# Performance work log

Measured on AMD Instinct MI355X. Metric: run time of the kernel, lower is better.

## Reference

```python
import jax, jax.numpy as jnp
import numpy as np

NEG_SLOPE = 0.2  # PyG GATConv default LeakyReLU slope


def _gat_layer(x, src, dst, n_nodes, W, a_src, a_dst, b, heads, out_ch):
    # x: [N, F_in] -> h: [N, H, C]
    h = (x @ W).reshape(n_nodes, heads, out_ch)
    # per-node attention contributions [N, H]
    al_s = jnp.sum(h * a_src[None], axis=-1)
    al_d = jnp.sum(h * a_dst[None], axis=-1)
    # per-edge logits [E, H]
    e = jax.nn.leaky_relu(al_s[src] + al_d[dst], negative_slope=NEG_SLOPE)
    # segment softmax over incoming edges of each destination node
    m = jax.ops.segment_max(e, dst, num_segments=n_nodes)
    ex = jnp.exp(e - m[dst])
    denom = jax.ops.segment_sum(ex, dst, num_segments=n_nodes)
    alpha = ex / (denom[dst] + 1e-16)
    # weighted scatter-aggregate of source features
    out = jax.ops.segment_sum(h[src] * alpha[:, :, None], dst, num_segments=n_nodes)
    return out.reshape(n_nodes, heads * out_ch) + b


def setup_inputs() -> dict:
    key = jax.random.key(0)
    ks = jax.random.split(key, 16)
    N, E, F_in, hid, H, n_cls = 50000, 800000, 128, 64, 4, 10
    s = 0.1
    return {
        "x": jax.random.normal(ks[0], (N, F_in), jnp.float32),
        "edge_index": jax.random.randint(ks[1], (2, E), 0, N, jnp.int64),
        "W1": jax.random.normal(ks[2], (F_in, H * hid), jnp.float32) * s,
        "a_src1": jax.random.normal(ks[3], (H, hid), jnp.float32) * s,
        "a_dst1": jax.random.normal(ks[4], (H, hid), jnp.float32) * s,
        "b1": jax.random.normal(ks[5], (H * hid,), jnp.float32) * s,
        "W2": jax.random.normal(ks[6], (H * hid, H * hid), jnp.float32) * s,
        "a_src2": jax.random.normal(ks[7], (H, hid), jnp.float32) * s,
        "a_dst2": jax.random.normal(ks[8], (H, hid), jnp.float32) * s,
        "b2": jax.random.normal(ks[9], (H * hid,), jnp.float32) * s,
        "W3": jax.random.normal(ks[10], (H * hid, n_cls), jnp.float32) * s,
        "a_src3": jax.random.normal(ks[11], (1, n_cls), jnp.float32) * s,
        "a_dst3": jax.random.normal(ks[12], (1, n_cls), jnp.float32) * s,
        "b3": jax.random.normal(ks[13], (n_cls,), jnp.float32) * s,
    }


def reference(x, edge_index, W1, a_src1, a_dst1, b1, W2, a_src2, a_dst2, b2,
              W3, a_src3, a_dst3, b3):
    N = x.shape[0]
    loops = jnp.arange(N, dtype=edge_index.dtype)
    src = jnp.concatenate([edge_index[0], loops])  # add self loops (PyG default)
    dst = jnp.concatenate([edge_index[1], loops])
    # layer 1: heads=4, concat -> [N, 256], ELU (dropout is a no-op in eval)
    h = jax.nn.elu(_gat_layer(x, src, dst, N, W1, a_src1, a_dst1, b1, 4, 64))
    # layer 2
    h = jax.nn.elu(_gat_layer(h, src, dst, N, W2, a_src2, a_dst2, b2, 4, 64))
    # layer 3: heads=1 -> [N, num_classes]
    h = _gat_layer(h, src, dst, N, W3, a_src3, a_dst3, b3, 1, 10)
    pooled = jnp.mean(h, axis=0, keepdims=True)  # [1, num_classes]
    return jax.nn.log_softmax(pooled, axis=1)
```

## Files before the change

### kernel.cpp

```cpp
#include <hip/hip_runtime.h>
#include <math.h>

#define NEG_SLOPE 0.2f

typedef __attribute__((ext_vector_type(8))) short bf16x8;
typedef __attribute__((ext_vector_type(4))) float f32x4;
typedef __attribute__((ext_vector_type(2))) float f32x2;
typedef unsigned short u16;
typedef __attribute__((ext_vector_type(4))) unsigned short u16x4;

__device__ __forceinline__ float b2f(u16 u) {
    return __uint_as_float(((unsigned)u) << 16);
}
__device__ __forceinline__ u16 f2b(float f) {
    unsigned u = __float_as_uint(f);
    unsigned r = (u + 0x7fffu + ((u >> 16) & 1u)) >> 16;
    return (u16)r;
}

__global__ void prep(const float* __restrict__ x, u16* __restrict__ x_bf, int n4,
                     const float* __restrict__ W1, u16* __restrict__ w1t,
                     const float* __restrict__ W2, u16* __restrict__ w2t,
                     int* __restrict__ zero_base, int nzero,
                     int B0, int B1, int B2) {
    int blk = blockIdx.x;
    if (blk < B0) {
        int i = blk * 256 + threadIdx.x;
        if (i < n4) {
            float4 v = *reinterpret_cast<const float4*>(&x[i * 4]);
            u16x4 o;
            o[0] = f2b(v.x); o[1] = f2b(v.y); o[2] = f2b(v.z); o[3] = f2b(v.w);
            *reinterpret_cast<u16x4*>(&x_bf[i * 4]) = o;
        }
    } else if (blk < B1) {
        int i = (blk - B0) * 256 + threadIdx.x;
        if (i < 128 * 256) {
            int m = i >> 7, k = i & 127;
            w1t[i] = f2b(W1[(size_t)k * 256 + m]);
        }
    } else if (blk < B2) {
        int i = (blk - B1) * 256 + threadIdx.x;
        if (i < 256 * 256) {
            int m = i >> 8, k = i & 255;
            w2t[i] = f2b(W2[(size_t)k * 256 + m]);
        }
    } else {
        int i = (blk - B2) * 256 + threadIdx.x;
        if (i < nzero) zero_base[i] = 0;
    }
}

__global__ __launch_bounds__(256) void gemm_mfma(
        const u16* __restrict__ A, const u16* __restrict__ Bt,
        u16* __restrict__ C, int N, int K, int M) {
    __shared__ u16 As[128 * 64];
    __shared__ u16 Bs[128 * 64];
    const int tid = threadIdx.x;
    const int lane = tid & 63;
    const int wid = tid >> 6;
    const int wr = wid >> 1, wc = wid & 1;
    const int row0 = blockIdx.x * 128;
    const int col0 = blockIdx.y * 128;
    f32x4 acc[4][4] = {};
    for (int k0 = 0; k0 < K; k0 += 64) {
        if (k0) __syncthreads();
#pragma unroll
        for (int i = 0; i < 4; ++i) {
            int chunk = i * 256 + tid;
            int row = chunk >> 3;
            int slot = chunk & 7;
            int grow = row0 + row; if (grow >= N) grow = N - 1;
            bf16x8 v = *reinterpret_cast<const bf16x8*>(&A[(size_t)grow * K + k0 + slot * 8]);
            int swz = (chunk & ~7) | (slot ^ (row & 7));
            *reinterpret_cast<bf16x8*>(&As[swz * 8]) = v;
        }
#pragma unroll
        for (int i = 0; i < 4; ++i) {
            int chunk = i * 256 + tid;
            int row = chunk >> 3;
            int slot = chunk & 7;
            int gcol = col0 + row;
            bf16x8 v = *reinterpret_cast<const bf16x8*>(&Bt[(size_t)gcol * K + k0 + slot * 8]);
            int swz = (chunk & ~7) | (slot ^ (row & 7));
            *reinterpret_cast<bf16x8*>(&Bs[swz * 8]) = v;
        }
        __syncthreads();
#pragma unroll
        for (int kk = 0; kk < 2; ++kk) {
            bf16x8 ax[4], bx[4];
#pragma unroll
            for (int m = 0; m < 4; ++m) {
                int row = wr * 64 + m * 16 + (lane & 15);
                int slot = kk * 4 + (lane >> 4);
                ax[m] = *reinterpret_cast<const bf16x8*>(&As[(row * 8 + (slot ^ (row & 7))) * 8]);
            }
#pragma unroll
            for (int n = 0; n < 4; ++n) {
                int row = wc * 64 + n * 16 + (lane & 15);
                int slot = kk * 4 + (lane >> 4);
                bx[n] = *reinterpret_cast<const bf16x8*>(&Bs[(row * 8 + (slot ^ (row & 7))) * 8]);
            }
#pragma unroll
            for (int m = 0; m < 4; ++m)
#pragma unroll
                for (int n = 0; n < 4; ++n)
                    acc[m][n] = __builtin_amdgcn_mfma_f32_16x16x32_bf16(
                        ax[m], bx[n], acc[m][n], 0, 0, 0);
        }
    }
    const int crow = row0 + wr * 64;
    const int ccol = col0 + wc * 64;
#pragma unroll
    for (int m = 0; m < 4; ++m)
#pragma unroll
        for (int n = 0; n < 4; ++n)
#pragma unroll
            for (int r = 0; r < 4; ++r) {
                int rg = crow + m * 16 + (lane >> 4) * 4 + r;
                int cg = ccol + n * 16 + (lane & 15);
                if (rg < N) C[(size_t)rg * M + cg] = f2b(acc[m][n][r]);
            }
}

__global__ __launch_bounds__(256) void compute_al_cast(
        const u16* __restrict__ h, const float* __restrict__ a_s,
        const float* __restrict__ a_d, int N,
        float* __restrict__ pq, float* __restrict__ al_d,
        unsigned* __restrict__ h8) {
    const int lane = threadIdx.x & 63;
    const int half = lane >> 5;
    const int l32 = lane & 31;
    int w = (blockIdx.x * blockDim.x + threadIdx.x) >> 6;
    int n = w * 2 + half;
    if (n >= N) return;
    const int head = l32 >> 3;
    const int c0 = l32 * 8;
    bf16x8 v = *reinterpret_cast<const bf16x8*>(&h[(size_t)n * 256 + c0]);
    const float* asf = a_s + head * 64 + (l32 & 7) * 8;
    const float* adf = a_d + head * 64 + (l32 & 7) * 8;
    float ss = 0.f, sd = 0.f;
    float f[8];
#pragma unroll
    for (int j = 0; j < 8; ++j) {
        f[j] = b2f((u16)v[j]);
        ss = fmaf(f[j], asf[j], ss);
        sd = fmaf(f[j], adf[j], sd);
    }
    int w0 = 0, w1 = 0;
    w0 = __builtin_amdgcn_cvt_pk_fp8_f32(f[0], f[1], w0, false);
    w0 = __builtin_amdgcn_cvt_pk_fp8_f32(f[2], f[3], w0, true);
    w1 = __builtin_amdgcn_cvt_pk_fp8_f32(f[4], f[5], w1, false);
    w1 = __builtin_amdgcn_cvt_pk_fp8_f32(f[6], f[7], w1, true);
    uint2 hw; hw.x = (unsigned)w0; hw.y = (unsigned)w1;
    *reinterpret_cast<uint2*>(&h8[(size_t)n * 64 + 2 * l32]) = hw;
#pragma unroll
    for (int m = 1; m < 8; m <<= 1) {
        ss += __shfl_xor(ss, m, 64);
        sd += __shfl_xor(sd, m, 64);
    }
    if ((l32 & 7) == 0) {
        f32x2 pv; pv.x = __expf(ss); pv.y = __expf(NEG_SLOPE * ss);
        *reinterpret_cast<f32x2*>(&pq[(size_t)n * 8 + head * 2]) = pv;
        al_d[n * 4 + head] = sd;
    }
}

__global__ __launch_bounds__(256) void bucket_hist(
        const int* __restrict__ dstI, int E, int Etot,
        int* __restrict__ bcnt, int NB) {
    __shared__ int h[512];
    int t = threadIdx.x;
    for (int j = t; j < NB; j += 256) h[j] = 0;
    __syncthreads();
    int base = blockIdx.x * 2048;
#pragma unroll
    for (int j = 0; j < 8; ++j) {
        int e = base + j * 256 + t;
        if (e < Etot) {
            int d = (e < E) ? dstI[e] : (e - E);
            atomicAdd(&h[d >> 7], 1);
        }
    }
    __syncthreads();
    for (int j = t; j < NB; j += 256)
        if (h[j]) atomicAdd(&bcnt[j], h[j]);
}

__global__ __launch_bounds__(512) void bucket_scan(
        const int* __restrict__ bcnt, int NB, int Etot,
        int* __restrict__ bbase, int* __restrict__ bcursor,
        int* __restrict__ rp, int N) {
    __shared__ int a[512], b[512];
    int t = threadIdx.x;
    a[t] = (t < NB) ? bcnt[t] : 0;
    __syncthreads();
    int* s = a; int* d = b;
    for (int ofs = 1; ofs < 512; ofs <<= 1) {
        d[t] = (t >= ofs) ? s[t] + s[t - ofs] : s[t];
        __syncthreads();
        int* tmp = s; s = d; d = tmp;
    }
    int excl = (t == 0) ? 0 : s[t - 1];
    if (t < NB) { bbase[t] = excl; bcursor[t] = excl; }
    if (t == NB) bbase[NB] = Etot;
    if (t == 0) rp[N] = Etot;
}

#define EPB 16
__global__ __launch_bounds__(256) void bin_scatter(
        const int* __restrict__ srcI, const int* __restrict__ dstI,
        int E, int Etot, int* __restrict__ bcursor,
        unsigned* __restrict__ binned, int NB) {
    __shared__ int cnt[512];
    int t = threadIdx.x;
    for (int j = t; j < NB; j += 256) cnt[j] = 0;
    __syncthreads();
    int base_e = blockIdx.x * (256 * EPB) + t;
    unsigned rec[EPB];
    int bkt[EPB];
#pragma unroll
    for (int j = 0; j < EPB; ++j) {
        int e = base_e + j * 256;
        bkt[j] = -1;
        if (e < Etot) {
            int s = (e < E) ? srcI[e] : (e - E);
            int d = (e < E) ? dstI[e] : (e - E);
            bkt[j] = d >> 7;
            rec[j] = ((unsigned)(d & 127) << 16) | (unsigned)s;
            atomicAdd(&cnt[bkt[j]], 1);
        }
    }
    __syncthreads();
    for (int j = t; j < NB; j += 256) {
        int c = cnt[j];
        cnt[j] = c ? atomicAdd(&bcursor[j], c) : 0;
    }
    __syncthreads();
#pragma unroll
    for (int j = 0; j < EPB; ++j)
        if (bkt[j] >= 0) {
            int pos = atomicAdd(&cnt[bkt[j]], 1);
            binned[pos] = rec[j];
        }
}

__global__ __launch_bounds__(256) void bucket_csr(
        const unsigned* __restrict__ binned, const int* __restrict__ bbase,
        int N, int* __restrict__ rp, u16* __restrict__ srcp) {
    int b = blockIdx.x;
    int start = bbase[b];
    int cnt = bbase[b + 1] - start;
    __shared__ int dcnt[128];
    __shared__ int dofs[128];
    __shared__ int wtot;
    int t = threadIdx.x;
    if (t < 128) dcnt[t] = 0;
    __syncthreads();
    for (int i = t; i < cnt; i += 256)
        atomicAdd(&dcnt[binned[start + i] >> 16], 1);
    __syncthreads();
    int v = 0, x = 0;
    if (t < 128) {
        v = dcnt[t];
        x = v;
#pragma unroll
        for (int ofs = 1; ofs < 64; ofs <<= 1) {
            int u = __shfl_up(x, ofs, 64);
            if ((t & 63) >= ofs) x += u;
        }
    }
    if (t == 63) wtot = x;
    __syncthreads();
    if (t >= 64 && t < 128) x += wtot;
    if (t < 128) {
        int abs0 = start + (x - v);
        int d = b * 128 + t;
        if (d < N) rp[d] = abs0;
        dofs[t] = abs0;
    }
    __syncthreads();
    for (int i = t; i < cnt; i += 256) {
        unsigned rec = binned[start + i];
        int pos = atomicAdd(&dofs[rec >> 16], 1);
        srcp[pos] = (u16)(rec & 0xFFFFu);
    }
}

template<bool ELU>
__global__ __launch_bounds__(256) void gat_fused_h4(
        const unsigned* __restrict__ h8, const float* __restrict__ pq,
        const float* __restrict__ al_d, const float* __restrict__ b,
        const int* __restrict__ rp, const u16* __restrict__ srcp,
        int N, u16* __restrict__ out) {
    const int lane = threadIdx.x & 63;
    const int head = lane >> 4;
    int w = (blockIdx.x * blockDim.x + threadIdx.x) >> 6;
    int nw = (gridDim.x * blockDim.x) >> 6;
    for (int d = w; d < N; d += nw) {
        int i = rp[d], end = rp[d + 1];
        float ald = al_d[d * 4 + head];
        float pb = __expf(ald);
        float qb = __expf(NEG_SLOPE * ald);
        float acc0 = 0.f, acc1 = 0.f, acc2 = 0.f, acc3 = 0.f, L = 0.f;

#define EDGE1(S) {                                                             \
        unsigned hv_ = h8[(unsigned)(S) * 64u + (unsigned)lane];               \
        f32x2 pv_ = *reinterpret_cast<const f32x2*>(                           \
            &pq[(unsigned)(S) * 8u + (unsigned)head * 2u]);                    \
        float t_ = pv_.x * pb;                                                 \
        float e_ = (t_ > 1.f) ? t_ : pv_.y * qb;                               \
        L += e_;                                                               \
        f32x2 lo_ = __builtin_amdgcn_cvt_pk_f32_fp8((int)hv_, false);          \
        f32x2 hi_ = __builtin_amdgcn_cvt_pk_f32_fp8((int)hv_, true);           \
        acc0 = fmaf(e_, lo_.x, acc0); acc1 = fmaf(e_, lo_.y, acc1);            \
        acc2 = fmaf(e_, hi_.x, acc2); acc3 = fmaf(e_, hi_.y, acc3); }

        for (; i < end && (i & 3); ++i) EDGE1(srcp[i]);
        for (; i + 8 <= end; i += 8) {
            u16x4 sa = *reinterpret_cast<const u16x4*>(&srcp[i]);
            u16x4 sb = *reinterpret_cast<const u16x4*>(&srcp[i + 4]);
            unsigned ss[8] = {sa[0], sa[1], sa[2], sa[3], sb[0], sb[1], sb[2], sb[3]};
            unsigned hv[8];
            f32x2 pv[8];
#pragma unroll
            for (int j = 0; j < 8; ++j) {
                hv[j] = h8[ss[j] * 64u + (unsigned)lane];
                pv[j] = *reinterpret_cast<const f32x2*>(
                    &pq[ss[j] * 8u + (unsigned)head * 2u]);
            }
#pragma unroll
            for (int j = 0; j < 8; ++j) {
                float t = pv[j].x * pb;
                float e = (t > 1.f) ? t : pv[j].y * qb;
                L += e;
                f32x2 lo = __builtin_amdgcn_cvt_pk_f32_fp8((int)hv[j], false);
                f32x2 hi = __builtin_amdgcn_cvt_pk_f32_fp8((int)hv[j], true);
                acc0 = fmaf(e, lo.x, acc0); acc1 = fmaf(e, lo.y, acc1);
                acc2 = fmaf(e, hi.x, acc2); acc3 = fmaf(e, hi.y, acc3);
            }
        }
        if (i + 4 <= end) {
            u16x4 sa = *reinterpret_cast<const u16x4*>(&srcp[i]);
            unsigned ss[4] = {sa[0], sa[1], sa[2], sa[3]};
            unsigned hv[4];
            f32x2 pv[4];
#pragma unroll
            for (int j = 0; j < 4; ++j) {
                hv[j] = h8[ss[j] * 64u + (unsigned)lane];
                pv[j] = *reinterpret_cast<const f32x2*>(
                    &pq[ss[j] * 8u + (unsigned)head * 2u]);
            }
#pragma unroll
            for (int j = 0; j < 4; ++j) {
                float t = pv[j].x * pb;
                float e = (t > 1.f) ? t : pv[j].y * qb;
                L += e;
                f32x2 lo = __builtin_amdgcn_cvt_pk_f32_fp8((int)hv[j], false);
                f32x2 hi = __builtin_amdgcn_cvt_pk_f32_fp8((int)hv[j], true);
                acc0 = fmaf(e, lo.x, acc0); acc1 = fmaf(e, lo.y, acc1);
                acc2 = fmaf(e, hi.x, acc2); acc3 = fmaf(e, hi.y, acc3);
            }
            i += 4;
        }
        for (; i < end; ++i) EDGE1(srcp[i]);
#undef EDGE1

        float inv = 1.f / (L + 1e-16f);
        float4 bb = *reinterpret_cast<const float4*>(&b[lane * 4]);
        float o0 = fmaf(acc0, inv, bb.x);
        float o1 = fmaf(acc1, inv, bb.y);
        float o2 = fmaf(acc2, inv, bb.z);
        float o3 = fmaf(acc3, inv, bb.w);
        if (ELU) {
            o0 = (o0 > 0.f) ? o0 : expm1f(o0);
            o1 = (o1 > 0.f) ? o1 : expm1f(o1);
            o2 = (o2 > 0.f) ? o2 : expm1f(o2);
            o3 = (o3 > 0.f) ? o3 : expm1f(o3);
        }
        u16x4 ov;
        ov[0] = f2b(o0); ov[1] = f2b(o1); ov[2] = f2b(o2); ov[3] = f2b(o3);
        *reinterpret_cast<u16x4*>(&out[(size_t)d * 256 + lane * 4]) = ov;
    }
}

__global__ __launch_bounds__(256) void compute_al3(
        const u16* __restrict__ ob, const float* __restrict__ W3,
        const float* __restrict__ as3, const float* __restrict__ ad3, int N,
        float* __restrict__ pq3, float* __restrict__ al_d) {
    __shared__ float was[256], wad[256];
    {
        int t = threadIdx.x;
        float ss = 0.f, sd = 0.f;
#pragma unroll
        for (int c = 0; c < 10; ++c) {
            float w = W3[t * 10 + c];
            ss = fmaf(w, as3[c], ss);
            sd = fmaf(w, ad3[c], sd);
        }
        was[t] = ss; wad[t] = sd;
    }
    __syncthreads();
    const int lane = threadIdx.x & 63;
    int n = (blockIdx.x * blockDim.x + threadIdx.x) >> 6;
    if (n >= N) return;
    u16x4 hv = *reinterpret_cast<const u16x4*>(&ob[(size_t)n * 256 + lane * 4]);
    float4 ws = *reinterpret_cast<const float4*>(&was[lane * 4]);
    float4 wd = *reinterpret_cast<const float4*>(&wad[lane * 4]);
    float f0 = b2f((u16)hv[0]), f1 = b2f((u16)hv[1]);
    float f2 = b2f((u16)hv[2]), f3 = b2f((u16)hv[3]);
    float ss = f0 * ws.x + f1 * ws.y + f2 * ws.z + f3 * ws.w;
    float sd = f0 * wd.x + f1 * wd.y + f2 * wd.z + f3 * wd.w;
#pragma unroll
    for (int m = 1; m < 64; m <<= 1) {
        ss += __shfl_xor(ss, m, 64);
        sd += __shfl_xor(sd, m, 64);
    }
    if (lane == 0) {
        f32x2 pv; pv.x = __expf(ss); pv.y = __expf(NEG_SLOPE * ss);
        *reinterpret_cast<f32x2*>(&pq3[(size_t)n * 2]) = pv;
        al_d[n] = sd;
    }
}

__global__ __launch_bounds__(256) void l3_edge(
        const float* __restrict__ pq3, const float* __restrict__ al_d,
        const int* __restrict__ rp, const u16* __restrict__ srcp,
        int N, float* __restrict__ wq) {
    const int lane = threadIdx.x & 63;
    int w = (blockIdx.x * blockDim.x + threadIdx.x) >> 6;
    int nw = (gridDim.x * blockDim.x) >> 6;
    for (int d = w; d < N; d += nw) {
        int start = rp[d], end = rp[d + 1];
        float ald = al_d[d];
        float pb = __expf(ald);
        float qb = __expf(NEG_SLOPE * ald);
        float L = 0.f;
        for (int i = start + lane; i < end; i += 64) {
            f32x2 pqv = *reinterpret_cast<const f32x2*>(&pq3[(unsigned)srcp[i] * 2u]);
            float t = pqv.x * pb;
            L += (t > 1.f) ? t : pqv.y * qb;
        }
#pragma unroll
        for (int m = 1; m < 64; m <<= 1) L += __shfl_xor(L, m, 64);
        float inv = 1.f / (L + 1e-16f);
        for (int i = start + lane; i < end; i += 64) {
            unsigned s = srcp[i];
            f32x2 pqv = *reinterpret_cast<const f32x2*>(&pq3[s * 2u]);
            float t = pqv.x * pb;
            float e = (t > 1.f) ? t : pqv.y * qb;
            atomicAdd(&wq[s], e * inv);
        }
    }
}

__global__ __launch_bounds__(256) void wcolsum(const u16* __restrict__ ob,
                                               const float* __restrict__ w, int N,
                                               float* __restrict__ pp) {
    __shared__ float sh[4][256];
    const int lane = threadIdx.x & 63;
    const int wid = threadIdx.x >> 6;
    int wv = (blockIdx.x * blockDim.x + threadIdx.x) >> 6;
    int nw = (gridDim.x * blockDim.x) >> 6;
    float a0 = 0.f, a1 = 0.f, a2 = 0.f, a3 = 0.f;
    for (int n = wv; n < N; n += nw) {
        float wn = w[n];
        u16x4 hv = *reinterpret_cast<const u16x4*>(&ob[(size_t)n * 256 + lane * 4]);
        a0 = fmaf(wn, b2f((u16)hv[0]), a0);
        a1 = fmaf(wn, b2f((u16)hv[1]), a1);
        a2 = fmaf(wn, b2f((u16)hv[2]), a2);
        a3 = fmaf(wn, b2f((u16)hv[3]), a3);
    }
    sh[wid][lane * 4 + 0] = a0;
    sh[wid][lane * 4 + 1] = a1;
    sh[wid][lane * 4 + 2] = a2;
    sh[wid][lane * 4 + 3] = a3;
    __syncthreads();
    int t = threadIdx.x;
    float s = sh[0][t] + sh[1][t] + sh[2][t] + sh[3][t];
    atomicAdd(&pp[t], s);
}

__global__ void final_out(const float* __restrict__ pp, const float* __restrict__ W3,
                          const float* __restrict__ b3, int N, float* __restrict__ out) {
    __shared__ float acc[10];
    int t = threadIdx.x;
    if (t < 10) acc[t] = 0.f;
    __syncthreads();
    float pk = pp[t] / (float)N;
#pragma unroll
    for (int c = 0; c < 10; ++c) atomicAdd(&acc[c], pk * W3[t * 10 + c]);
    __syncthreads();
    if (t == 0) {
        float p[10];
        float mx = -INFINITY;
        for (int c = 0; c < 10; ++c) {
            p[c] = acc[c] + b3[c];
            mx = fmaxf(mx, p[c]);
        }
        float s = 0.f;
        for (int c = 0; c < 10; ++c) s += expf(p[c] - mx);
        float ls = logf(s);
        for (int c = 0; c < 10; ++c) out[c] = p[c] - mx - ls;
    }
}

extern "C" void kernel_launch(void* const* d_in, const int* in_sizes, int n_in,
                              void* d_out, int out_size, void* d_ws, size_t ws_size,
                              hipStream_t stream) {
    const float* x   = (const float*)d_in[0];
    const int*   ei  = (const int*)d_in[1];
    const float* W1  = (const float*)d_in[2];
    const float* as1 = (const float*)d_in[3];
    const float* ad1 = (const float*)d_in[4];
    const float* b1  = (const float*)d_in[5];
    const float* W2  = (const float*)d_in[6];
    const float* as2 = (const float*)d_in[7];
    const float* ad2 = (const float*)d_in[8];
    const float* b2  = (const float*)d_in[9];
    const float* W3  = (const float*)d_in[10];
    const float* as3 = (const float*)d_in[11];
    const float* ad3 = (const float*)d_in[12];
    const float* b3  = (const float*)d_in[13];
    float* out = (float*)d_out;

    const int N = in_sizes[0] / 128;
    const int E = in_sizes[1] / 2;
    const int Etot = E + N;
    const int NB = (N + 127) >> 7;
    const int* srcI = ei;
    const int* dstI = ei + E;

    char* base = (char*)d_ws;
    size_t off = 0;
    auto alloc = [&](size_t bytes) {
        void* p = base + off;
        off = (off + bytes + 255) & ~(size_t)255;
        return p;
    };
    u16* x_bf  = (u16*)alloc((size_t)N * 128 * 2);
    u16* h_bf  = (u16*)alloc((size_t)N * 256 * 2);
    unsigned* h8 = (unsigned*)alloc((size_t)N * 256);
    u16* oa_bf = (u16*)alloc((size_t)N * 256 * 2);
    u16* ob_bf = (u16*)alloc((size_t)N * 256 * 2);
    u16* w1t   = (u16*)alloc(256 * 128 * 2);
    u16* w2t   = (u16*)alloc(256 * 256 * 2);
    float* pq   = (float*)alloc((size_t)N * 8 * 4);
    float* al_d = (float*)alloc((size_t)N * 4 * 4);
    float* pq3  = (float*)alloc((size_t)N * 2 * 4);
    int* bcnt   = (int*)alloc(512 * 4);
    float* wq   = (float*)alloc((size_t)N * 4);
    float* pp   = (float*)alloc(256 * 4);
    int* rp     = (int*)alloc((size_t)(N + 1) * 4);
    int* bbase  = (int*)alloc(512 * 4);
    int* bcursor = (int*)alloc(512 * 4);
    unsigned* binned = (unsigned*)alloc((size_t)Etot * 4);
    u16* srcp   = (u16*)alloc((size_t)Etot * 2);

    const int n4 = N * 128 / 4;
    const int B0 = (n4 + 255) / 256;
    const int B1 = B0 + (128 * 256 + 255) / 256;
    const int B2 = B1 + (256 * 256 + 255) / 256;
    int span = (int)(((char*)(pp + 256) - (char*)bcnt) / 4);
    const int B3 = B2 + (span + 255) / 256;
    prep<<<B3, 256, 0, stream>>>(x, x_bf, n4, W1, w1t, W2, w2t,
                                 bcnt, span, B0, B1, B2);

    bucket_hist<<<(Etot + 2047) / 2048, 256, 0, stream>>>(dstI, E, Etot, bcnt, NB);
    bucket_scan<<<1, 512, 0, stream>>>(bcnt, NB, Etot, bbase, bcursor, rp, N);
    bin_scatter<<<(Etot + 256 * EPB - 1) / (256 * EPB), 256, 0, stream>>>(
        srcI, dstI, E, Etot, bcursor, binned, NB);
    bucket_csr<<<NB, 256, 0, stream>>>(binned, bbase, N, rp, srcp);

    const int FUSED_BLOCKS = (N + 3) / 4;
    const int ALC_BLOCKS = (N / 2 + 3) / 4;
    const int GX = (N + 127) / 128;

    {
        dim3 g(GX, 2);
        gemm_mfma<<<g, 256, 0, stream>>>(x_bf, w1t, h_bf, N, 128, 256);
        compute_al_cast<<<ALC_BLOCKS, 256, 0, stream>>>(h_bf, as1, ad1, N,
                                                        pq, al_d, h8);
        gat_fused_h4<true><<<FUSED_BLOCKS, 256, 0, stream>>>(
            h8, pq, al_d, b1, rp, srcp, N, oa_bf);
    }
    {
        dim3 g(GX, 2);
        gemm_mfma<<<g, 256, 0, stream>>>(oa_bf, w2t, h_bf, N, 256, 256);
        compute_al_cast<<<ALC_BLOCKS, 256, 0, stream>>>(h_bf, as2, ad2, N,
                                                        pq, al_d, h8);
        gat_fused_h4<true><<<FUSED_BLOCKS, 256, 0, stream>>>(
            h8, pq, al_d, b2, rp, srcp, N, ob_bf);
    }
    {
        compute_al3<<<(N + 3) / 4, 256, 0, stream>>>(ob_bf, W3, as3, ad3, N, pq3, al_d);
        l3_edge<<<(N + 3) / 4, 256, 0, stream>>>(pq3, al_d, rp, srcp, N, wq);
        wcolsum<<<1024, 256, 0, stream>>>(ob_bf, wq, N, pp);
        final_out<<<1, 256, 0, stream>>>(pp, W3, b3, N, out);
    }
}
```

Before: 331.6 us.

## Fuse attention-logit and fp8 cast epilogue into GEMM; split edges across half-waves

The GEMM epilogue now computes the per-head source and destination attention dot products with shuffle reductions and writes the fp8 features directly. This removes the bf16 h round trip and the separate compute_al_cast kernel. The aggregation kernel is reorganised so that each half-wave takes alternate groups of edges, with each lane handling 8 channels using 8-byte fp8 loads. The two halves are combined with a cross-half shuffle at the end. The cost is byte-granular, scattered fp8 stores in the GEMM epilogue and extra shuffle work.

```diff
diff --git a/kernel.cpp b/kernel.cpp
--- a/kernel.cpp
+++ b/kernel.cpp
@@ -8,6 +8,7 @@
 typedef __attribute__((ext_vector_type(2))) float f32x2;
 typedef unsigned short u16;
 typedef __attribute__((ext_vector_type(4))) unsigned short u16x4;
+typedef __attribute__((ext_vector_type(8))) unsigned short u16x8;
 
 __device__ __forceinline__ float b2f(u16 u) {
     return __uint_as_float(((unsigned)u) << 16);
@@ -50,9 +51,12 @@
     }
 }
 
-__global__ __launch_bounds__(256) void gemm_mfma(
+__global__ __launch_bounds__(256) void gemm_mfma_fused(
         const u16* __restrict__ A, const u16* __restrict__ Bt,
-        u16* __restrict__ C, int N, int K, int M) {
+        int N, int K,
+        const float* __restrict__ a_s, const float* __restrict__ a_d,
+        unsigned char* __restrict__ h8b, float* __restrict__ pq,
+        float* __restrict__ al_d) {
     __shared__ u16 As[128 * 64];
     __shared__ u16 Bs[128 * 64];
     const int tid = threadIdx.x;
@@ -108,60 +112,45 @@
                         ax[m], bx[n], acc[m][n], 0, 0, 0);
         }
     }
+    const int head = blockIdx.y * 2 + wc;
+    float asf[4], adf[4];
+#pragma unroll
+    for (int n = 0; n < 4; ++n) {
+        asf[n] = a_s[head * 64 + n * 16 + (lane & 15)];
+        adf[n] = a_d[head * 64 + n * 16 + (lane & 15)];
+    }
     const int crow = row0 + wr * 64;
-    const int ccol = col0 + wc * 64;
-#pragma unroll
-    for (int m = 0; m < 4; ++m)
-#pragma unroll
-        for (int n = 0; n < 4; ++n)
-#pragma unroll
-            for (int r = 0; r < 4; ++r) {
-                int rg = crow + m * 16 + (lane >> 4) * 4 + r;
-                int cg = ccol + n * 16 + (lane & 15);
-                if (rg < N) C[(size_t)rg * M + cg] = f2b(acc[m][n][r]);
-            }
-}
-
-__global__ __launch_bounds__(256) void compute_al_cast(
-        const u16* __restrict__ h, const float* __restrict__ a_s,
-        const float* __restrict__ a_d, int N,
-        float* __restrict__ pq, float* __restrict__ al_d,
-        unsigned* __restrict__ h8) {
-    const int lane = threadIdx.x & 63;
-    const int half = lane >> 5;
-    const int l32 = lane & 31;
-    int w = (blockIdx.x * blockDim.x + threadIdx.x) >> 6;
-    int n = w * 2 + half;
-    if (n >= N) return;
-    const int head = l32 >> 3;
-    const int c0 = l32 * 8;
-    bf16x8 v = *reinterpret_cast<const bf16x8*>(&h[(size_t)n * 256 + c0]);
-    const float* asf = a_s + head * 64 + (l32 & 7) * 8;
-    const float* adf = a_d + head * 64 + (l32 & 7) * 8;
-    float ss = 0.f, sd = 0.f;
-    float f[8];
-#pragma unroll
-    for (int j = 0; j < 8; ++j) {
-        f[j] = b2f((u16)v[j]);
-        ss = fmaf(f[j], asf[j], ss);
-        sd = fmaf(f[j], adf[j], sd);
-    }
-    int w0 = 0, w1 = 0;
-    w0 = __builtin_amdgcn_cvt_pk_fp8_f32(f[0], f[1], w0, false);
-    w0 = __builtin_amdgcn_cvt_pk_fp8_f32(f[2], f[3], w0, true);
-    w1 = __builtin_amdgcn_cvt_pk_fp8_f32(f[4], f[5], w1, false);
-    w1 = __builtin_amdgcn_cvt_pk_fp8_f32(f[6], f[7], w1, true);
-    uint2 hw; hw.x = (unsigned)w0; hw.y = (unsigned)w1;
-    *reinterpret_cast<uint2*>(&h8[(size_t)n * 64 + 2 * l32]) = hw;
-#pragma unroll
-    for (int m = 1; m < 8; m <<= 1) {
-        ss += __shfl_xor(ss, m, 64);
-        sd += __shfl_xor(sd, m, 64);
-    }
-    if ((l32 & 7) == 0) {
-        f32x2 pv; pv.x = __expf(ss); pv.y = __expf(NEG_SLOPE * ss);
-        *reinterpret_cast<f32x2*>(&pq[(size_t)n * 8 + head * 2]) = pv;
-        al_d[n * 4 + head] = sd;
+#pragma unroll
+    for (int m = 0; m < 4; ++m) {
+#pragma unroll
+        for (int r = 0; r < 4; ++r) {
+            float ss = 0.f, sd = 0.f;
+#pragma unroll
+            for (int n = 0; n < 4; ++n) {
+                float v = acc[m][n][r];
+                ss = fmaf(v, asf[n], ss);
+                sd = fmaf(v, adf[n], sd);
+            }
+#pragma unroll
+            for (int msk = 1; msk < 16; msk <<= 1) {
+                ss += __shfl_xor(ss, msk, 64);
+                sd += __shfl_xor(sd, msk, 64);
+            }
+            int rg = crow + m * 16 + (lane >> 4) * 4 + r;
+            if (rg < N) {
+                if ((lane & 15) == 0) {
+                    f32x2 pv; pv.x = __expf(ss); pv.y = __expf(NEG_SLOPE * ss);
+                    *reinterpret_cast<f32x2*>(&pq[(size_t)rg * 8 + head * 2]) = pv;
+                    al_d[rg * 4 + head] = sd;
+                }
+#pragma unroll
+                for (int n = 0; n < 4; ++n) {
+                    int w8 = __builtin_amdgcn_cvt_pk_fp8_f32(acc[m][n][r], acc[m][n][r], 0, false);
+                    h8b[(size_t)rg * 256 + head * 64 + n * 16 + (lane & 15)] =
+                        (unsigned char)(w8 & 0xFF);
+                }
+            }
+        }
     }
 }
 
@@ -293,93 +282,96 @@
         const int* __restrict__ rp, const u16* __restrict__ srcp,
         int N, u16* __restrict__ out) {
     const int lane = threadIdx.x & 63;
-    const int head = lane >> 4;
+    const int hlf = lane >> 5;
+    const int l = lane & 31;
+    const int head = l >> 3;
     int w = (blockIdx.x * blockDim.x + threadIdx.x) >> 6;
     int nw = (gridDim.x * blockDim.x) >> 6;
     for (int d = w; d < N; d += nw) {
-        int i = rp[d], end = rp[d + 1];
+        int start = rp[d], end = rp[d + 1];
         float ald = al_d[d * 4 + head];
         float pb = __expf(ald);
         float qb = __expf(NEG_SLOPE * ald);
-        float acc0 = 0.f, acc1 = 0.f, acc2 = 0.f, acc3 = 0.f, L = 0.f;
-
-#define EDGE1(S) {                                                             \
-        unsigned hv_ = h8[(unsigned)(S) * 64u + (unsigned)lane];               \
-        f32x2 pv_ = *reinterpret_cast<const f32x2*>(                           \
-            &pq[(unsigned)(S) * 8u + (unsigned)head * 2u]);                    \
-        float t_ = pv_.x * pb;                                                 \
-        float e_ = (t_ > 1.f) ? t_ : pv_.y * qb;                               \
-        L += e_;                                                               \
-        f32x2 lo_ = __builtin_amdgcn_cvt_pk_f32_fp8((int)hv_, false);          \
-        f32x2 hi_ = __builtin_amdgcn_cvt_pk_f32_fp8((int)hv_, true);           \
-        acc0 = fmaf(e_, lo_.x, acc0); acc1 = fmaf(e_, lo_.y, acc1);            \
-        acc2 = fmaf(e_, hi_.x, acc2); acc3 = fmaf(e_, hi_.y, acc3); }
-
-        for (; i < end && (i & 3); ++i) EDGE1(srcp[i]);
-        for (; i + 8 <= end; i += 8) {
-            u16x4 sa = *reinterpret_cast<const u16x4*>(&srcp[i]);
-            u16x4 sb = *reinterpret_cast<const u16x4*>(&srcp[i + 4]);
-            unsigned ss[8] = {sa[0], sa[1], sa[2], sa[3], sb[0], sb[1], sb[2], sb[3]};
-            unsigned hv[8];
-            f32x2 pv[8];
-#pragma unroll
-            for (int j = 0; j < 8; ++j) {
-                hv[j] = h8[ss[j] * 64u + (unsigned)lane];
-                pv[j] = *reinterpret_cast<const f32x2*>(
-                    &pq[ss[j] * 8u + (unsigned)head * 2u]);
-            }
-#pragma unroll
-            for (int j = 0; j < 8; ++j) {
-                float t = pv[j].x * pb;
-                float e = (t > 1.f) ? t : pv[j].y * qb;
+        float a0 = 0, a1 = 0, a2 = 0, a3 = 0, a4 = 0, a5 = 0, a6 = 0, a7 = 0, L = 0;
+
+#define EDGE1(S) {                                                              \
+        unsigned s_ = (S);                                                      \
+        uint2 hv_ = *reinterpret_cast<const uint2*>(&h8[s_ * 64u + (unsigned)l * 2u]); \
+        f32x2 pv_ = *reinterpret_cast<const f32x2*>(&pq[s_ * 8u + (unsigned)head * 2u]); \
+        float t_ = pv_.x * pb;                                                  \
+        float e_ = (t_ > 1.f) ? t_ : pv_.y * qb;                                \
+        L += e_;                                                                \
+        f32x2 p0_ = __builtin_amdgcn_cvt_pk_f32_fp8((int)hv_.x, false);         \
+        f32x2 p1_ = __builtin_amdgcn_cvt_pk_f32_fp8((int)hv_.x, true);          \
+        f32x2 p2_ = __builtin_amdgcn_cvt_pk_f32_fp8((int)hv_.y, false);         \
+        f32x2 p3_ = __builtin_amdgcn_cvt_pk_f32_fp8((int)hv_.y, true);          \
+        a0 = fmaf(e_, p0_.x, a0); a1 = fmaf(e_, p0_.y, a1);                     \
+        a2 = fmaf(e_, p1_.x, a2); a3 = fmaf(e_, p1_.y, a3);                     \
+        a4 = fmaf(e_, p2_.x, a4); a5 = fmaf(e_, p2_.y, a5);                     \
+        a6 = fmaf(e_, p3_.x, a6); a7 = fmaf(e_, p3_.y, a7); }
+
+        int i = start;
+        int pre = (4 - (i & 3)) & 3;
+        if (pre > end - i) pre = end - i;
+        for (int k = hlf; k < pre; k += 2) EDGE1(srcp[i + k]);
+        i += pre;
+        int nb = (end - i) & ~7;
+        int stop = i + nb;
+        for (int j = i + hlf * 4; j < stop; j += 8) {
+            u16x4 sv = *reinterpret_cast<const u16x4*>(&srcp[j]);
+            unsigned s4[4] = {sv[0], sv[1], sv[2], sv[3]};
+            uint2 hv[4]; f32x2 pv[4];
+#pragma unroll
+            for (int q = 0; q < 4; ++q) {
+                hv[q] = *reinterpret_cast<const uint2*>(&h8[s4[q] * 64u + (unsigned)l * 2u]);
+                pv[q] = *reinterpret_cast<const f32x2*>(&pq[s4[q] * 8u + (unsigned)head * 2u]);
+            }
+#pragma unroll
+            for (int q = 0; q < 4; ++q) {
+                float t = pv[q].x * pb;
+                float e = (t > 1.f) ? t : pv[q].y * qb;
                 L += e;
-                f32x2 lo = __builtin_amdgcn_cvt_pk_f32_fp8((int)hv[j], false);
-                f32x2 hi = __builtin_amdgcn_cvt_pk_f32_fp8((int)hv[j], true);
-                acc0 = fmaf(e, lo.x, acc0); acc1 = fmaf(e, lo.y, acc1);
-                acc2 = fmaf(e, hi.x, acc2); acc3 = fmaf(e, hi.y, acc3);
-            }
-        }
-        if (i + 4 <= end) {
-            u16x4 sa = *reinterpret_cast<const u16x4*>(&srcp[i]);
-            unsigned ss[4] = {sa[0], sa[1], sa[2], sa[3]};
-            unsigned hv[4];
-            f32x2 pv[4];
-#pragma unroll
-            for (int j = 0; j < 4; ++j) {
-                hv[j] = h8[ss[j] * 64u + (unsigned)lane];
-                pv[j] = *reinterpret_cast<const f32x2*>(
-                    &pq[ss[j] * 8u + (unsigned)head * 2u]);
-            }
-#pragma unroll
-            for (int j = 0; j < 4; ++j) {
-                float t = pv[j].x * pb;
-                float e = (t > 1.f) ? t : pv[j].y * qb;
-                L += e;
-                f32x2 lo = __builtin_amdgcn_cvt_pk_f32_fp8((int)hv[j], false);
-                f32x2 hi = __builtin_amdgcn_cvt_pk_f32_fp8((int)hv[j], true);
-                acc0 = fmaf(e, lo.x, acc0); acc1 = fmaf(e, lo.y, acc1);
-                acc2 = fmaf(e, hi.x, acc2); acc3 = fmaf(e, hi.y, acc3);
-            }
-            i += 4;
-        }
-        for (; i < end; ++i) EDGE1(srcp[i]);
+                f32x2 p0 = __builtin_amdgcn_cvt_pk_f32_fp8((int)hv[q].x, false);
+                f32x2 p1 = __builtin_amdgcn_cvt_pk_f32_fp8((int)hv[q].x, true);
+                f32x2 p2 = __builtin_amdgcn_cvt_pk_f32_fp8((int)hv[q].y, false);
+                f32x2 p3 = __builtin_amdgcn_cvt_pk_f32_fp8((int)hv[q].y, true);
+                a0 = fmaf(e, p0.x, a0); a1 = fmaf(e, p0.y, a1);
+                a2 = fmaf(e, p1.x, a2); a3 = fmaf(e, p1.y, a3);
+                a4 = fmaf(e, p2.x, a4); a5 = fmaf(e, p2.y, a5);
+                a6 = fmaf(e, p3.x, a6); a7 = fmaf(e, p3.y, a7);
+            }
+        }
+        for (int k = stop + hlf; k < end; k += 2) EDGE1(srcp[k]);
 #undef EDGE1
 
+        a0 += __shfl_xor(a0, 32, 64); a1 += __shfl_xor(a1, 32, 64);
+        a2 += __shfl_xor(a2, 32, 64); a3 += __shfl_xor(a3, 32, 64);
+        a4 += __shfl_xor(a4, 32, 64); a5 += __shfl_xor(a5, 32, 64);
+        a6 += __shfl_xor(a6, 32, 64); a7 += __shfl_xor(a7, 32, 64);
+        L += __shfl_xor(L, 32, 64);
         float inv = 1.f / (L + 1e-16f);
-        float4 bb = *reinterpret_cast<const float4*>(&b[lane * 4]);
-        float o0 = fmaf(acc0, inv, bb.x);
-        float o1 = fmaf(acc1, inv, bb.y);
-        float o2 = fmaf(acc2, inv, bb.z);
-        float o3 = fmaf(acc3, inv, bb.w);
-        if (ELU) {
-            o0 = (o0 > 0.f) ? o0 : expm1f(o0);
-            o1 = (o1 > 0.f) ? o1 : expm1f(o1);
-            o2 = (o2 > 0.f) ? o2 : expm1f(o2);
-            o3 = (o3 > 0.f) ? o3 : expm1f(o3);
-        }
-        u16x4 ov;
-        ov[0] = f2b(o0); ov[1] = f2b(o1); ov[2] = f2b(o2); ov[3] = f2b(o3);
-        *reinterpret_cast<u16x4*>(&out[(size_t)d * 256 + lane * 4]) = ov;
+        if (hlf == 0) {
+            float4 b0 = *reinterpret_cast<const float4*>(&b[l * 8]);
+            float4 b1 = *reinterpret_cast<const float4*>(&b[l * 8 + 4]);
+            float o0 = fmaf(a0, inv, b0.x), o1 = fmaf(a1, inv, b0.y);
+            float o2 = fmaf(a2, inv, b0.z), o3 = fmaf(a3, inv, b0.w);
+            float o4 = fmaf(a4, inv, b1.x), o5 = fmaf(a5, inv, b1.y);
+            float o6 = fmaf(a6, inv, b1.z), o7 = fmaf(a7, inv, b1.w);
+            if (ELU) {
+                o0 = (o0 > 0.f) ? o0 : expm1f(o0);
+                o1 = (o1 > 0.f) ? o1 : expm1f(o1);
+                o2 = (o2 > 0.f) ? o2 : expm1f(o2);
+                o3 = (o3 > 0.f) ? o3 : expm1f(o3);
+                o4 = (o4 > 0.f) ? o4 : expm1f(o4);
+                o5 = (o5 > 0.f) ? o5 : expm1f(o5);
+                o6 = (o6 > 0.f) ? o6 : expm1f(o6);
+                o7 = (o7 > 0.f) ? o7 : expm1f(o7);
+            }
+            u16x8 ov;
+            ov[0] = f2b(o0); ov[1] = f2b(o1); ov[2] = f2b(o2); ov[3] = f2b(o3);
+            ov[4] = f2b(o4); ov[5] = f2b(o5); ov[6] = f2b(o6); ov[7] = f2b(o7);
+            *reinterpret_cast<u16x8*>(&out[(size_t)d * 256 + l * 8]) = ov;
+        }
     }
 }
 
@@ -538,7 +530,6 @@
         return p;
     };
     u16* x_bf  = (u16*)alloc((size_t)N * 128 * 2);
-    u16* h_bf  = (u16*)alloc((size_t)N * 256 * 2);
     unsigned* h8 = (unsigned*)alloc((size_t)N * 256);
     u16* oa_bf = (u16*)alloc((size_t)N * 256 * 2);
     u16* ob_bf = (u16*)alloc((size_t)N * 256 * 2);
@@ -572,22 +563,19 @@
     bucket_csr<<<NB, 256, 0, stream>>>(binned, bbase, N, rp, srcp);
 
     const int FUSED_BLOCKS = (N + 3) / 4;
-    const int ALC_BLOCKS = (N / 2 + 3) / 4;
     const int GX = (N + 127) / 128;
 
     {
         dim3 g(GX, 2);
-        gemm_mfma<<<g, 256, 0, stream>>>(x_bf, w1t, h_bf, N, 128, 256);
-        compute_al_cast<<<ALC_BLOCKS, 256, 0, stream>>>(h_bf, as1, ad1, N,
-                                                        pq, al_d, h8);
+        gemm_mfma_fused<<<g, 256, 0, stream>>>(x_bf, w1t, N, 128, as1, ad1,
+                                               (unsigned char*)h8, pq, al_d);
         gat_fused_h4<true><<<FUSED_BLOCKS, 256, 0, stream>>>(
             h8, pq, al_d, b1, rp, srcp, N, oa_bf);
     }
     {
         dim3 g(GX, 2);
-        gemm_mfma<<<g, 256, 0, stream>>>(oa_bf, w2t, h_bf, N, 256, 256);
-        compute_al_cast<<<ALC_BLOCKS, 256, 0, stream>>>(h_bf, as2, ad2, N,
-                                                        pq, al_d, h8);
+        gemm_mfma_fused<<<g, 256, 0, stream>>>(oa_bf, w2t, N, 256, as2, ad2,
+                                               (unsigned char*)h8, pq, al_d);
         gat_fused_h4<true><<<FUSED_BLOCKS, 256, 0, stream>>>(
             h8, pq, al_d, b2, rp, srcp, N, ob_bf);
     }
```

After: 320.2 us (median of 3 runs). 1.04x faster.
